# Kernel optimization log

Hardware: AMD Instinct MI355X
Metric: run time of the kernel (lower is better)

Reference implementation:

```python
import jax, jax.numpy as jnp
import numpy as np

B, M, D = 512, 96, 512
H = 8            # num_heads
DH = D // H      # head dim
NC = 3           # num_clusters
BETA = 5
MEM = 1024       # memory_size
EPS = 1e-8


def _l2norm(x, axis=-1):
    # torch F.cosine_similarity clamps each norm at eps=1e-8
    n = jnp.linalg.norm(x, axis=axis, keepdims=True)
    return x / jnp.maximum(n, EPS)


def _dynamic_clustering(sims):
    # sims: (B, M). Sort descending, split into NC equal groups,
    # per-group mean and (unbiased) std. (dynamic_clustering is not
    # defined in the source repo; this is the assumed implementation.)
    s = -jnp.sort(-sims, axis=1)               # descending
    g = s.reshape(B, NC, M // NC)
    means = g.mean(axis=-1)                    # (B, NC)
    stds = jnp.std(g, axis=-1, ddof=1)         # (B, NC)
    return means, stds


def setup_inputs() -> dict:
    key = jax.random.key(0)
    ks = jax.random.split(key, 6)
    vis_global = jax.random.normal(ks[0], (B, D), dtype=jnp.float32)
    text_features = jax.random.normal(ks[1], (B, M, D), dtype=jnp.float32)
    scale = 1.0 / np.sqrt(D)
    in_proj_w = jax.random.normal(ks[2], (3 * D, D), dtype=jnp.float32) * scale
    in_proj_b = jnp.zeros((3 * D,), dtype=jnp.float32)
    out_proj_w = jax.random.normal(ks[3], (D, D), dtype=jnp.float32) * scale
    out_proj_b = jnp.zeros((D,), dtype=jnp.float32)
    text_memory = jax.random.normal(ks[4], (MEM, D), dtype=jnp.float32)
    tau_p_log = jnp.log(jnp.asarray(0.1, dtype=jnp.float32))
    tau_n_log = jnp.log(jnp.asarray(0.05, dtype=jnp.float32))
    return dict(vis_global=vis_global, text_features=text_features,
                in_proj_w=in_proj_w, in_proj_b=in_proj_b,
                out_proj_w=out_proj_w, out_proj_b=out_proj_b,
                text_memory=text_memory, tau_p_log=tau_p_log, tau_n_log=tau_n_log)


def reference(vis_global, text_features, in_proj_w, in_proj_b,
              out_proj_w, out_proj_b, text_memory, tau_p_log, tau_n_log):
    # --- dynamic clustering over visual-text cosine sims ---
    sims = jnp.einsum('bd,bmd->bm', _l2norm(vis_global), _l2norm(text_features))
    means, stds = _dynamic_clustering(sims)
    cluster_scores = means / (stds + 1e-6)     # (B, NC)

    # --- MultiheadAttention: 1-token query, M-token key/value ---
    wq, wk, wv = in_proj_w[:D], in_proj_w[D:2 * D], in_proj_w[2 * D:]
    bq, bk, bv = in_proj_b[:D], in_proj_b[D:2 * D], in_proj_b[2 * D:]
    q = (vis_global @ wq.T + bq).reshape(B, H, DH)              # (B,H,DH)
    k = (text_features @ wk.T + bk).reshape(B, M, H, DH)        # (B,M,H,DH)
    v = (text_features @ wv.T + bv).reshape(B, M, H, DH)
    attn = jax.nn.softmax(jnp.einsum('bhd,bmhd->bhm', q, k) / np.sqrt(DH), axis=-1)
    ctx = jnp.einsum('bhm,bmhd->bhd', attn, v).reshape(B, D)
    corrected = ctx @ out_proj_w.T + out_proj_b                 # (B, D)

    tau_p = jnp.exp(tau_p_log)
    tau_n = jnp.exp(tau_n_log)
    pos_sim = jnp.sum(_l2norm(vis_global) * _l2norm(corrected), axis=-1)  # (B,)

    # memory-bank scatter (ptr starts at 0) + negatives, all detached
    corr_sg = jax.lax.stop_gradient(corrected)
    mem = text_memory.at[0:B].set(corr_sg)
    all_negs = jnp.concatenate([jnp.roll(corr_sg, 1, axis=0), mem], axis=0)  # (B+MEM, D)

    neg_sims = _l2norm(vis_global) @ _l2norm(all_negs).T        # (B, B+MEM)
    hard_negs, _ = jax.lax.top_k(neg_sims, BETA)                # (B, BETA)

    pos_term = jnp.exp(pos_sim / tau_p)
    neg_terms = jnp.exp(hard_negs / tau_n).sum(axis=1)
    loss = -jnp.mean(jnp.log(pos_term / (pos_term + neg_terms + 1e-8)))
    return loss, corrected, cluster_scores
```

## Files before the change

kernel.cpp:

```cpp
#include <hip/hip_runtime.h>
#include <math.h>

typedef unsigned short u16;
typedef unsigned int u32;
typedef __attribute__((ext_vector_type(8))) short short8;
typedef __attribute__((ext_vector_type(8))) _Float16 half8;
typedef __attribute__((ext_vector_type(4))) float f32x4;

#define EPS 1e-8f

__device__ inline float bf2f(u16 u) {
    union { u32 i; float f; } v; v.i = ((u32)u) << 16; return v.f;
}
__device__ inline u16 f2bf(float f) {
    union { float f; u32 u; } v; v.f = f;
    u32 r = v.u + 0x7fffu + ((v.u >> 16) & 1u);
    return (u16)(r >> 16);
}
__device__ inline u16 f2h(float f) {
    _Float16 h = (_Float16)f;
    union { _Float16 hh; u16 u; } v; v.hh = h; return v.u;
}
__device__ inline u32 pack2(float a, float b) {
    return (u32)f2bf(a) | ((u32)f2bf(b) << 16);
// ... 11 lines not shown
    #pragma unroll
    for (int kk = 0; kk < 16; kk++) {
        int c = c0 + kk * 32;
        *(uint4*)&As[srow * 520 + c] = *(const uint4*)&Ag[(size_t)srow * lda + c];
    }
}
__device__ __forceinline__ void mfma_k512(const u16* __restrict__ As,
                                          const u16* __restrict__ Bs,
                                          f32x4 (&acc)[2][2]) {
    const int t = threadIdx.x, lane = t & 63, w = t >> 6;
    const int wm = (w >> 1) * 32, wn = (w & 1) * 32;
    const int l16 = lane & 15, quad = lane >> 4;
    #pragma unroll
    for (int ks = 0; ks < 16; ks++) {
        short8 af[2], bfr[2];
        #pragma unroll
        for (int i = 0; i < 2; i++)
            af[i] = *(const short8*)&As[(wm + i * 16 + l16) * 520 + ks * 32 + quad * 8];
        #pragma unroll
        for (int j = 0; j < 2; j++)
            bfr[j] = *(const short8*)&Bs[(wn + j * 16 + l16) * 520 + ks * 32 + quad * 8];
        #pragma unroll
        for (int i = 0; i < 2; i++)
            #pragma unroll
            for (int j = 0; j < 2; j++)
                acc[i][j] = __builtin_amdgcn_mfma_f32_16x16x32_bf16(af[i], bfr[j], acc[i][j], 0, 0, 0);
    }
}

__global__ __launch_bounds__(256) void prep(const float* __restrict__ vis,
                                            const float* __restrict__ ipw,
                                            const float* __restrict__ opw,
                                            const float* __restrict__ tm,
                                            float* __restrict__ vis_n,
                                            u16* __restrict__ vis_nb,
                                            u16* __restrict__ vis_b,
                                            u16* __restrict__ wqb,
                                            u16* __restrict__ wvb,
                                            u16* __restrict__ wob,
                                            u16* __restrict__ negsb,
                                            u16* __restrict__ wkT,
                                            u16* __restrict__ woT,
                                            float* __restrict__ corrSS,
                                            float* __restrict__ loss0)
{
    int bid = blockIdx.x;
    int t = threadIdx.x;
    if (bid >= 1088) {
        __shared__ __align__(16) u16 T[64 * 72];
        int idx = bid - 1088;
        int a = idx >> 3, cb = idx & 7;
        int r = t >> 2, c0 = (t & 3) * 16;
        #pragma unroll
        for (int q = 0; q < 4; q++) {
            float4 v = *(const float4*)&opw[(size_t)(a * 64 + r) * 512 + cb * 64 + c0 + q * 4];
            T[(c0 + q * 4 + 0) * 72 + r] = f2bf(v.x);
            T[(c0 + q * 4 + 1) * 72 + r] = f2bf(v.y);
            T[(c0 + q * 4 + 2) * 72 + r] = f2bf(v.z);
            T[(c0 + q * 4 + 3) * 72 + r] = f2bf(v.w);
        }
        __syncthreads();
        int j = t >> 2, ch = (t & 3) * 16;
        *(uint4*)&woT[(size_t)(cb * 64 + j) * 512 + a * 64 + ch]     = *(const uint4*)&T[j * 72 + ch];
        *(uint4*)&woT[(size_t)(cb * 64 + j) * 512 + a * 64 + ch + 8] = *(const uint4*)&T[j * 72 + ch + 8];
        return;
    }
    if (bid >= 1024) {
        __shared__ __align__(16) u16 T[64 * 72];
        int idx = bid - 1024;
        int a = idx >> 3, cb = idx & 7;
        const float* wk = ipw + 262144;
        int r = t >> 2, c0 = (t & 3) * 16;
        #pragma unroll
        for (int q = 0; q < 4; q++) {
            float4 v = *(const float4*)&wk[(size_t)(a * 64 + r) * 512 + cb * 64 + c0 + q * 4];
            T[(c0 + q * 4 + 0) * 72 + r] = f2h(v.x);
            T[(c0 + q * 4 + 1) * 72 + r] = f2h(v.y);
            T[(c0 + q * 4 + 2) * 72 + r] = f2h(v.z);
            T[(c0 + q * 4 + 3) * 72 + r] = f2h(v.w);
        }
        __syncthreads();
        int j = t >> 2, ch = (t & 3) * 16;
        *(uint4*)&wkT[(size_t)(cb * 64 + j) * 512 + a * 64 + ch]     = *(const uint4*)&T[j * 72 + ch];
        *(uint4*)&wkT[(size_t)(cb * 64 + j) * 512 + a * 64 + ch + 8] = *(const uint4*)&T[j * 72 + ch + 8];
        return;
    }
    if (bid >= 896) {
        int wave = t >> 6, lane = t & 63;
        int j = 512 + (bid - 896) * 4 + wave;
        const float* row = tm + (size_t)(j - 512) * 512 + lane * 8;
        float4 x0 = *(const float4*)row;
        float4 x1 = *(const float4*)(row + 4);
        float ss = x0.x*x0.x + x0.y*x0.y + x0.z*x0.z + x0.w*x0.w
                 + x1.x*x1.x + x1.y*x1.y + x1.z*x1.z + x1.w*x1.w;
        ss = wave_sum(ss);
        float inv = 1.0f / fmaxf(sqrtf(ss), EPS);
        uint4 pk;
        pk.x = pack2(x0.x*inv, x0.y*inv); pk.y = pack2(x0.z*inv, x0.w*inv);
        pk.z = pack2(x1.x*inv, x1.y*inv); pk.w = pack2(x1.z*inv, x1.w*inv);
        *(uint4*)(negsb + (size_t)j * 512 + lane * 8) = pk;
        return;
    }
    if (bid >= 128) {
        int i = ((bid - 128) * 256 + t) * 4;
        const float* src; u16* dst; int j;
        if (i < 262144)      { j = i;          src = ipw + j;          dst = wqb + j; }
        else if (i < 524288) { j = i - 262144; src = ipw + 524288 + j; dst = wvb + j; }
        else                 { j = i - 524288; src = opw + j;          dst = wob + j; }
        float4 v = *(const float4*)src;
        uint2 pk; pk.x = pack2(v.x, v.y); pk.y = pack2(v.z, v.w);
        *(uint2*)dst = pk;
        return;
    }
    if (bid == 0) {
        if (t == 0) loss0[0] = 0.0f;
        corrSS[t] = 0.0f;
        corrSS[t + 256] = 0.0f;
    }
    int wave = t >> 6, lane = t & 63;
    int b = bid * 4 + wave;
    const float* row = vis + (size_t)b * 512 + lane * 8;
    float4 x0 = *(const float4*)row;
    float4 x1 = *(const float4*)(row + 4);
    uint4 rk;
    rk.x = pack2(x0.x, x0.y); rk.y = pack2(x0.z, x0.w);
    rk.z = pack2(x1.x, x1.y); rk.w = pack2(x1.z, x1.w);
    *(uint4*)(vis_b + (size_t)b * 512 + lane * 8) = rk;
    float ss = x0.x*x0.x + x0.y*x0.y + x0.z*x0.z + x0.w*x0.w
             + x1.x*x1.x + x1.y*x1.y + x1.z*x1.z + x1.w*x1.w;
    ss = wave_sum(ss);
    float inv = 1.0f / fmaxf(sqrtf(ss), EPS);
    float4 y0, y1;
    y0.x = x0.x*inv; y0.y = x0.y*inv; y0.z = x0.z*inv; y0.w = x0.w*inv;
    y1.x = x1.x*inv; y1.y = x1.y*inv; y1.z = x1.z*inv; y1.w = x1.w*inv;
    *(float4*)(vis_n + (size_t)b * 512 + lane * 8)     = y0;
    *(float4*)(vis_n + (size_t)b * 512 + lane * 8 + 4) = y1;
    uint4 pk;
    pk.x = pack2(y0.x, y0.y); pk.y = pack2(y0.z, y0.w);
    pk.z = pack2(y1.x, y1.y); pk.w = pack2(y1.z, y1.w);
    *(uint4*)(vis_nb + (size_t)b * 512 + lane * 8) = pk;
}

__global__ __launch_bounds__(256) void mid(const u16* __restrict__ visb,
                                           const u16* __restrict__ vis_nb,
                                           const u16* __restrict__ wqb,
                                           const float* __restrict__ ipb,
                                           const u16* __restrict__ wkT,
                                           u16* __restrict__ qkb,
                                           const u16* __restrict__ negsb,
                                           float* __restrict__ ns,
                                           const u16* __restrict__ woT,
                                           u16* __restrict__ G,
                                           const float* __restrict__ opb,
                                           float* __restrict__ vb,
                                           const float* __restrict__ vis_n)
{
    __shared__ __align__(16) u16 SM[3 * 64 * 72];
    const int bid = blockIdx.x;
    const int t = threadIdx.x, lane = t & 63, w = t >> 6;

    if (bid >= 192) {
        int idx = bid - 192;
        #pragma unroll 2
        for (int k = 0; k < 16; k++) {
            int b = idx * 64 + w * 16 + k;
            const float* vn = vis_n + (size_t)b * 512 + lane * 8;
            float4 a = *(const float4*)vn, c = *(const float4*)(vn + 4);
            const float* bo = opb + lane * 8;
            float4 b0 = *(const float4*)bo, b1 = *(const float4*)(bo + 4);
            float dt = a.x*b0.x + a.y*b0.y + a.z*b0.z + a.w*b0.w
                     + c.x*b1.x + c.y*b1.y + c.z*b1.z + c.w*b1.w;
            dt = wave_sum(dt);
            if (lane == 0) vb[b] = dt;
        }
        return;
    }

    const int wm = (w >> 1) * 32, wn = (w & 1) * 32;
    const int l16 = lane & 15, quad = lane >> 4;
    const int srow = t >> 3, scol = (t & 7) * 8;

    if (bid >= 64) {
        u16* As = SM;
        u16* Bs = SM + 4608;
        bool isG = (bid >= 128);
        int idx = bid - (isG ? 128 : 64);
        int m0 = (idx & 7) * 64, n0 = (idx >> 3) * 64;
        const u16* Bsrc = isG ? (woT + (size_t)n0 * 512)
                              : (negsb + (size_t)(512 + n0) * 512);
        f32x4 acc[2][2];
        for (int i = 0; i < 2; i++)
            for (int j = 0; j < 2; j++)
                for (int e = 0; e < 4; e++) acc[i][j][e] = 0.f;
        for (int ko = 0; ko < 512; ko += 64) {
            __syncthreads();
            #pragma unroll
            for (int i = 0; i < 2; i++) {
                int row = i * 32 + srow;
                *(uint4*)&As[row * 72 + scol] = *(const uint4*)&vis_nb[(size_t)(m0 + row) * 512 + ko + scol];
                *(uint4*)&Bs[row * 72 + scol] = *(const uint4*)&Bsrc[(size_t)row * 512 + ko + scol];
            }
            __syncthreads();
            #pragma unroll
            for (int ks = 0; ks < 2; ks++) {
                short8 af[2], bfr[2];
                #pragma unroll
                for (int i = 0; i < 2; i++)
                    af[i] = *(const short8*)&As[(wm + i * 16 + l16) * 72 + ks * 32 + quad * 8];
                #pragma unroll
                for (int j = 0; j < 2; j++)
                    bfr[j] = *(const short8*)&Bs[(wn + j * 16 + l16) * 72 + ks * 32 + quad * 8];
                #pragma unroll
                for (int i = 0; i < 2; i++)
                    #pragma unroll
                    for (int j = 0; j < 2; j++)
                        acc[i][j] = __builtin_amdgcn_mfma_f32_16x16x32_bf16(af[i], bfr[j], acc[i][j], 0, 0, 0);
            }
        }
        #pragma unroll
        for (int i = 0; i < 2; i++)
            #pragma unroll
            for (int j = 0; j < 2; j++)
                #pragma unroll
                for (int r = 0; r < 4; r++) {
                    int row = m0 + wm + i * 16 + quad * 4 + r;
                    int col = n0 + wn + j * 16 + l16;
                    if (isG) G[(size_t)row * 512 + col] = f2bf(acc[i][j][r]);
                    else     ns[(size_t)row * 1024 + 512 + col] = acc[i][j][r];
                }
        return;
    }

    u16* As = SM;
    u16* Bs = SM + 4608;
    u16* Qf = SM + 9216;
    const int m0 = (bid & 7) * 64, h = bid >> 3;

    f32x4 acc[2][2];
    for (int i = 0; i < 2; i++)
        for (int j = 0; j < 2; j++)
            for (int e = 0; e < 4; e++) acc[i][j][e] = 0.f;

    for (int ko = 0; ko < 512; ko += 64) {
        __syncthreads();
        #pragma unroll
        for (int i = 0; i < 2; i++) {
            int row = i * 32 + srow;
            *(uint4*)&As[row * 72 + scol] = *(const uint4*)&visb[(size_t)(m0 + row) * 512 + ko + scol];
            *(uint4*)&Bs[row * 72 + scol] = *(const uint4*)&wqb[(size_t)(h * 64 + row) * 512 + ko + scol];
        }
        __syncthreads();
        #pragma unroll
        for (int ks = 0; ks < 2; ks++) {
            short8 af[2], bfr[2];
            #pragma unroll
            for (int i = 0; i < 2; i++)
                af[i] = *(const short8*)&As[(wm + i * 16 + l16) * 72 + ks * 32 + quad * 8];
            #pragma unroll
            for (int j = 0; j < 2; j++)
                bfr[j] = *(const short8*)&Bs[(wn + j * 16 + l16) * 72 + ks * 32 + quad * 8];
            #pragma unroll
            for (int i = 0; i < 2; i++)
                #pragma unroll
                for (int j = 0; j < 2; j++)
                    acc[i][j] = __builtin_amdgcn_mfma_f32_16x16x32_bf16(af[i], bfr[j], acc[i][j], 0, 0, 0);
        }
    }
    #pragma unroll
    for (int i = 0; i < 2; i++)
        #pragma unroll
        for (int j = 0; j < 2; j++)
            #pragma unroll
            for (int r = 0; r < 4; r++) {
                int rl = wm + i * 16 + quad * 4 + r;
                int cl = wn + j * 16 + l16;
                Qf[rl * 72 + cl] = f2h(acc[i][j][r] + ipb[h * 64 + cl]);
            }
    for (int jt = 0; jt < 8; jt++) {
        __syncthreads();
        #pragma unroll
        for (int i = 0; i < 2; i++) {
            int row = i * 32 + srow;
            *(uint4*)&Bs[row * 72 + scol] = *(const uint4*)&wkT[(size_t)(jt * 64 + row) * 512 + h * 64 + scol];
        }
        __syncthreads();
        f32x4 a2[2][2];
        for (int i = 0; i < 2; i++)
            for (int j = 0; j < 2; j++)
                for (int e = 0; e < 4; e++) a2[i][j][e] = 0.f;
        #pragma unroll
        for (int ks = 0; ks < 2; ks++) {
            half8 af[2], bfr[2];
            #pragma unroll
            for (int i = 0; i < 2; i++)
                af[i] = *(const half8*)&Qf[(wm + i * 16 + l16) * 72 + ks * 32 + quad * 8];
            #pragma unroll
            for (int j = 0; j < 2; j++)
                bfr[j] = *(const half8*)&Bs[(wn + j * 16 + l16) * 72 + ks * 32 + quad * 8];
            #pragma unroll
            for (int i = 0; i < 2; i++)
                #pragma unroll
                for (int j = 0; j < 2; j++)
                    a2[i][j] = __builtin_amdgcn_mfma_f32_16x16x32_f16(af[i], bfr[j], a2[i][j], 0, 0, 0);
        }
        #pragma unroll
        for (int i = 0; i < 2; i++)
            #pragma unroll
            for (int j = 0; j < 2; j++)
                #pragma unroll
                for (int r = 0; r < 4; r++) {
                    int rb = m0 + wm + i * 16 + quad * 4 + r;
                    int cj = jt * 64 + wn + j * 16 + l16;
                    qkb[((size_t)rb * 8 + h) * 512 + cj] = f2bf(a2[i][j][r]);
                }
    }
}

__global__ __launch_bounds__(1024) void attn(const float* __restrict__ tf,
                                             const float* __restrict__ vis_n,
                                             const u16* __restrict__ qkb,
                                             u16* __restrict__ u_allb,
                                             float* __restrict__ out_cs)
{
    __shared__ __align__(16) u16 Xs[96 * 520];
    __shared__ __align__(16) u16 Qs[16 * 520];
    __shared__ __align__(16) u16 Ps[16 * 104];
    __shared__ float Sc[16 * 100];
    __shared__ float sm_[96], srt[96], linv[8];

    const int b = blockIdx.x;
    const int t = threadIdx.x, w = t >> 6, lane = t & 63;
    const int l16 = lane & 15, quad = lane >> 4;

    const float4* v4 = (const float4*)(vis_n + (size_t)b * 512 + lane * 8);
    float4 va = v4[0], vbv = v4[1];

    #pragma unroll
    for (int i = 0; i < 3; i++) {
        int m0r = w + i * 32;
        int m1r = m0r + 16;
        const float4* pa = (const float4*)(tf + ((size_t)b * 96 + m0r) * 512 + lane * 8);
        const float4* pb = (const float4*)(tf + ((size_t)b * 96 + m1r) * 512 + lane * 8);
        float4 a0 = pa[0], c0 = pa[1];
        float4 a1 = pb[0], c1 = pb[1];
        float ss0 = a0.x*a0.x + a0.y*a0.y + a0.z*a0.z + a0.w*a0.w
                  + c0.x*c0.x + c0.y*c0.y + c0.z*c0.z + c0.w*c0.w;
        float dt0 = a0.x*va.x + a0.y*va.y + a0.z*va.z + a0.w*va.w
                  + c0.x*vbv.x + c0.y*vbv.y + c0.z*vbv.z + c0.w*vbv.w;
        float ss1 = a1.x*a1.x + a1.y*a1.y + a1.z*a1.z + a1.w*a1.w
                  + c1.x*c1.x + c1.y*c1.y + c1.z*c1.z + c1.w*c1.w;
        float dt1 = a1.x*va.x + a1.y*va.y + a1.z*va.z + a1.w*va.w
                  + c1.x*vbv.x + c1.y*vbv.y + c1.z*vbv.z + c1.w*vbv.w;
        #pragma unroll
        for (int off = 32; off; off >>= 1) {
            ss0 += __shfl_xor(ss0, off, 64);
            dt0 += __shfl_xor(dt0, off, 64);
            ss1 += __shfl_xor(ss1, off, 64);
            dt1 += __shfl_xor(dt1, off, 64);
        }
        if (lane == 0) {
            sm_[m0r] = dt0 / fmaxf(sqrtf(ss0), EPS);
            sm_[m1r] = dt1 / fmaxf(sqrtf(ss1), EPS);
        }
        uint4 pk0, pk1;
        pk0.x = pack2(a0.x, a0.y); pk0.y = pack2(a0.z, a0.w);
        pk0.z = pack2(c0.x, c0.y); pk0.w = pack2(c0.z, c0.w);
        pk1.x = pack2(a1.x, a1.y); pk1.y = pack2(a1.z, a1.w);
        pk1.z = pack2(c1.x, c1.y); pk1.w = pack2(c1.z, c1.w);
        *(uint4*)&Xs[m0r * 520 + lane * 8] = pk0;
        *(uint4*)&Xs[m1r * 520 + lane * 8] = pk1;
    }
    if (w < 8) {
        *(uint4*)&Qs[w * 520 + lane * 8] = *(const uint4*)(qkb + ((size_t)b * 8 + w) * 512 + lane * 8);
    } else {
        uint4 z; z.x = 0; z.y = 0; z.z = 0; z.w = 0;
        *(uint4*)&Qs[w * 520 + lane * 8] = z;
    }
    __syncthreads();

    if (w < 6) {
        f32x4 acc;
        for (int e = 0; e < 4; e++) acc[e] = 0.f;
        #pragma unroll
        for (int ks = 0; ks < 16; ks++) {
            short8 a = *(const short8*)&Xs[(w * 16 + l16) * 520 + ks * 32 + quad * 8];
            short8 q = *(const short8*)&Qs[l16 * 520 + ks * 32 + quad * 8];
            acc = __builtin_amdgcn_mfma_f32_16x16x32_bf16(a, q, acc, 0, 0, 0);
        }
        #pragma unroll
        for (int r = 0; r < 4; r++)
            Sc[l16 * 100 + w * 16 + quad * 4 + r] = acc[r] * 0.125f;
    }
    __syncthreads();

    if (w < 8) {
        float e0 = __expf(Sc[w * 100 + lane]);
        float e1 = (lane < 32) ? __expf(Sc[w * 100 + 64 + lane]) : 0.f;
        float l = wave_sum(e0 + e1);
        Ps[w * 104 + lane] = f2bf(e0);
        if (lane < 32) Ps[w * 104 + 64 + lane] = f2bf(e1);
        if (lane == 0) linv[w] = 1.0f / l;
    } else {
        Ps[w * 104 + lane] = 0;
        if (lane < 40) Ps[w * 104 + 64 + lane] = 0;
    }
    if (t < 96) {
        float v = sm_[t]; int r = 0;
        for (int j = 0; j < 96; j++) {
            float u = sm_[j];
            r += (u > v) || (u == v && j < t);
        }
        srt[r] = v;
    }
    __syncthreads();

    #pragma unroll
    for (int jj = 0; jj < 2; jj++) {
        int n0 = (w * 2 + jj) * 16;
        f32x4 acc;
        for (int e = 0; e < 4; e++) acc[e] = 0.f;
        #pragma unroll
        for (int ks = 0; ks < 3; ks++) {
            short8 ap = *(const short8*)&Ps[l16 * 104 + ks * 32 + quad * 8];
            short8 bx;
            #pragma unroll
            for (int j = 0; j < 8; j++)
                bx[j] = (short)Xs[(ks * 32 + quad * 8 + j) * 520 + n0 + l16];
            acc = __builtin_amdgcn_mfma_f32_16x16x32_bf16(ap, bx, acc, 0, 0, 0);
        }
        if (quad < 2) {
            #pragma unroll
            for (int r = 0; r < 4; r++) {
                int h = quad * 4 + r;
                u_allb[((size_t)b * 8 + h) * 512 + n0 + l16] = f2bf(acc[r] * linv[h]);
            }
        }
    }
    if (t < 3) {
        float mean = 0.f;
        #pragma unroll 8
        for (int i = 0; i < 32; i++) mean += srt[t * 32 + i];
        mean *= (1.0f / 32.0f);
        float var = 0.f;
        #pragma unroll 8
        for (int i = 0; i < 32; i++) { float d = srt[t * 32 + i] - mean; var += d * d; }
        var *= (1.0f / 31.0f);
        out_cs[b * 3 + t] = mean / (sqrtf(var) + 1e-6f);
    }
}

__global__ __launch_bounds__(256) void ghead(const u16* __restrict__ u_allb,
                                             const u16* __restrict__ wvb,
                                             const float* __restrict__ bv,
                                             u16* __restrict__ ctxb)
{
    __shared__ __align__(16) u16 As[64 * 520];
    __shared__ __align__(16) u16 Bs[64 * 520];
    const int bid = blockIdx.x;
    const int m0 = (bid & 7) * 64, h = bid >> 3;
    const int t = threadIdx.x, lane = t & 63, w = t >> 6;
    const int wm = (w >> 1) * 32, wn = (w & 1) * 32;
    const int l16 = lane & 15, quad = lane >> 4;

    f32x4 acc[2][2];
    for (int i = 0; i < 2; i++)
        for (int j = 0; j < 2; j++)
            for (int e = 0; e < 4; e++) acc[i][j][e] = 0.f;

    stage64x512(u_allb + (size_t)m0 * 4096 + (size_t)h * 512, 4096, As);
    stage64x512(wvb + (size_t)h * 64 * 512, 512, Bs);
    __syncthreads();
    mfma_k512(As, Bs, acc);

    for (int i = 0; i < 2; i++) {
        int row = m0 + wm + i * 16 + quad * 4;
        for (int j = 0; j < 2; j++) {
            int col = wn + j * 16 + l16;
            float bb = bv[h * 64 + col];
            for (int r = 0; r < 4; r++)
                ctxb[(size_t)(row + r) * 512 + h * 64 + col] = f2bf(acc[i][j][r] + bb);
        }
    }
}

__global__ __launch_bounds__(256) void tail2(const u16* __restrict__ ctxb,
                                             const u16* __restrict__ wob,
                                             const float* __restrict__ bias,
                                             float* __restrict__ Cf,
                                             float* __restrict__ corrSS,
                                             const u16* __restrict__ G,
                                             const float* __restrict__ vb,
                                             float* __restrict__ ns)
{
    __shared__ __align__(16) u16 As[64 * 520];
    __shared__ __align__(16) u16 Bs[64 * 520];
    const int bid = blockIdx.x;
    const int t = threadIdx.x, lane = t & 63, w = t >> 6;
    const int wm = (w >> 1) * 32, wn = (w & 1) * 32;
    const int l16 = lane & 15, quad = lane >> 4;

    f32x4 acc[2][2];
    for (int i = 0; i < 2; i++)
        for (int j = 0; j < 2; j++)
            for (int e = 0; e < 4; e++) acc[i][j][e] = 0.f;

    if (bid < 64) {
        const int m0 = (bid & 7) * 64, n0 = (bid >> 3) * 64;
        stage64x512(ctxb + (size_t)m0 * 512, 512, As);
        stage64x512(wob + (size_t)n0 * 512, 512, Bs);
        __syncthreads();
        mfma_k512(As, Bs, acc);
        #pragma unroll
        for (int i = 0; i < 2; i++) {
// ... 111 lines not shown
        }
        if (lane == 0) {
            float pos = ns[(size_t)b * 1024 + b] * invn[b];
            float tp = expf(tau_p_log[0]);
            float p = expf(pos / tp);
            float term = logf(p / (p + nsum + 1e-8f));
            atomicAdd(out_loss, -term * (1.0f / 512.0f));
        }
    }
}

extern "C" void kernel_launch(void* const* d_in, const int* in_sizes, int n_in,
                              void* d_out, int out_size, void* d_ws, size_t ws_size,
                              hipStream_t stream) {
    const float* vis = (const float*)d_in[0];
    const float* tf  = (const float*)d_in[1];
    const float* ipw = (const float*)d_in[2];
    const float* ipb = (const float*)d_in[3];
    const float* opw = (const float*)d_in[4];
    const float* opb = (const float*)d_in[5];
    const float* tm  = (const float*)d_in[6];
    const float* tpl = (const float*)d_in[7];
    const float* tnl = (const float*)d_in[8];

    float* out       = (float*)d_out;
    float* out_loss  = out;
    float* out_corr  = out + 1;
    float* out_cs    = out + 1 + 512 * 512;

    char* p = (char*)d_ws;
    auto alloc = [&](size_t bytes) { char* r = p; p += (bytes + 255) & ~(size_t)255; return r; };
    float* vis_n  = (float*)alloc(512 * 512 * 4);
    u16*   vis_nb = (u16*)  alloc(512 * 512 * 2);
    u16*   vis_b  = (u16*)  alloc(512 * 512 * 2);
    u16*   wqb    = (u16*)  alloc(512 * 512 * 2);
    u16*   wvb    = (u16*)  alloc(512 * 512 * 2);
    u16*   wob    = (u16*)  alloc(512 * 512 * 2);
    u16*   wkT    = (u16*)  alloc(512 * 512 * 2);
    u16*   woT    = (u16*)  alloc(512 * 512 * 2);
    u16*   G      = (u16*)  alloc(512 * 512 * 2);
    u16*   qkb    = (u16*)  alloc((size_t)512 * 8 * 512 * 2);
    u16*   u_allb = (u16*)  alloc((size_t)512 * 8 * 512 * 2);
    u16*   ctxb   = (u16*)  alloc(512 * 512 * 2);
    u16*   negsb  = (u16*)  alloc(1024 * 512 * 2);
    float* ns     = (float*)alloc(512 * 1024 * 4);
    float* corrSS = (float*)alloc(512 * 4);
    float* vb     = (float*)alloc(512 * 4);

    const float* bv = ipb + 2 * 512;

    prep<<<1152, 256, 0, stream>>>(vis, ipw, opw, tm, vis_n, vis_nb, vis_b,
                                   wqb, wvb, wob, negsb, wkT, woT, corrSS, out_loss);
    mid<<<200, 256, 0, stream>>>(vis_b, vis_nb, wqb, ipb, wkT, qkb, negsb, ns,
                                 woT, G, opb, vb, vis_n);
    attn<<<512, 1024, 0, stream>>>(tf, vis_n, qkb, u_allb, out_cs);
    ghead<<<64, 256, 0, stream>>>(u_allb, wvb, bv, ctxb);
    tail2<<<128, 256, 0, stream>>>(ctxb, wob, opb, out_corr, corrSS, G, vb, ns);
    topk_loss<<<512, 256, 0, stream>>>(ns, corrSS, tpl, tnl, out_loss);
}
```

Before: 224.6 us.

## Fuse q/qk projection into prep and merge ghead with mid into one kernel

```diff
diff --git a/kernel.cpp b/kernel.cpp
--- a/kernel.cpp
+++ b/kernel.cpp
@@ -67,23 +67,23 @@
                                             const float* __restrict__ ipw,
                                             const float* __restrict__ opw,
                                             const float* __restrict__ tm,
+                                            const float* __restrict__ ipb,
                                             float* __restrict__ vis_n,
                                             u16* __restrict__ vis_nb,
-                                            u16* __restrict__ vis_b,
-                                            u16* __restrict__ wqb,
                                             u16* __restrict__ wvb,
                                             u16* __restrict__ wob,
                                             u16* __restrict__ negsb,
-                                            u16* __restrict__ wkT,
                                             u16* __restrict__ woT,
+                                            u16* __restrict__ qkb,
                                             float* __restrict__ corrSS,
                                             float* __restrict__ loss0)
 {
+    __shared__ __align__(16) u16 SMEM[3 * 64 * 72];
     int bid = blockIdx.x;
     int t = threadIdx.x;
-    if (bid >= 1088) {
-        __shared__ __align__(16) u16 T[64 * 72];
-        int idx = bid - 1088;
+    if (bid >= 832) {
+        u16* T = SMEM;
+        int idx = bid - 832;
         int a = idx >> 3, cb = idx & 7;
         int r = t >> 2, c0 = (t & 3) * 16;
         #pragma unroll
@@ -100,29 +100,9 @@
         *(uint4*)&woT[(size_t)(cb * 64 + j) * 512 + a * 64 + ch + 8] = *(const uint4*)&T[j * 72 + ch + 8];
         return;
     }
-    if (bid >= 1024) {
-        __shared__ __align__(16) u16 T[64 * 72];
-        int idx = bid - 1024;
-        int a = idx >> 3, cb = idx & 7;
-        const float* wk = ipw + 262144;
-        int r = t >> 2, c0 = (t & 3) * 16;
-        #pragma unroll
-        for (int q = 0; q < 4; q++) {
-            float4 v = *(const float4*)&wk[(size_t)(a * 64 + r) * 512 + cb * 64 + c0 + q * 4];
-            T[(c0 + q * 4 + 0) * 72 + r] = f2h(v.x);
-            T[(c0 + q * 4 + 1) * 72 + r] = f2h(v.y);
-            T[(c0 + q * 4 + 2) * 72 + r] = f2h(v.z);
-            T[(c0 + q * 4 + 3) * 72 + r] = f2h(v.w);
-        }
-        __syncthreads();
-        int j = t >> 2, ch = (t & 3) * 16;
-        *(uint4*)&wkT[(size_t)(cb * 64 + j) * 512 + a * 64 + ch]     = *(const uint4*)&T[j * 72 + ch];
-        *(uint4*)&wkT[(size_t)(cb * 64 + j) * 512 + a * 64 + ch + 8] = *(const uint4*)&T[j * 72 + ch + 8];
-        return;
-    }
-    if (bid >= 896) {
+    if (bid >= 704) {
         int wave = t >> 6, lane = t & 63;
-        int j = 512 + (bid - 896) * 4 + wave;
+        int j = 512 + (bid - 704) * 4 + wave;
         const float* row = tm + (size_t)(j - 512) * 512 + lane * 8;
         float4 x0 = *(const float4*)row;
         float4 x1 = *(const float4*)(row + 4);
@@ -136,63 +116,303 @@
         *(uint4*)(negsb + (size_t)j * 512 + lane * 8) = pk;
         return;
     }
-    if (bid >= 128) {
-        int i = ((bid - 128) * 256 + t) * 4;
-        const float* src; u16* dst; int j;
-        if (i < 262144)      { j = i;          src = ipw + j;          dst = wqb + j; }
-        else if (i < 524288) { j = i - 262144; src = ipw + 524288 + j; dst = wvb + j; }
-        else                 { j = i - 524288; src = opw + j;          dst = wob + j; }
-        float4 v = *(const float4*)src;
+    if (bid >= 448) {
+        int i = (bid - 448) * 1024 + t * 4;
+        float4 v = *(const float4*)(opw + i);
         uint2 pk; pk.x = pack2(v.x, v.y); pk.y = pack2(v.z, v.w);
-        *(uint2*)dst = pk;
-        return;
-    }
-    if (bid == 0) {
-        if (t == 0) loss0[0] = 0.0f;
-        corrSS[t] = 0.0f;
-        corrSS[t + 256] = 0.0f;
-    }
-    int wave = t >> 6, lane = t & 63;
-    int b = bid * 4 + wave;
-    const float* row = vis + (size_t)b * 512 + lane * 8;
-    float4 x0 = *(const float4*)row;
-    float4 x1 = *(const float4*)(row + 4);
-    uint4 rk;
-    rk.x = pack2(x0.x, x0.y); rk.y = pack2(x0.z, x0.w);
-    rk.z = pack2(x1.x, x1.y); rk.w = pack2(x1.z, x1.w);
-    *(uint4*)(vis_b + (size_t)b * 512 + lane * 8) = rk;
-    float ss = x0.x*x0.x + x0.y*x0.y + x0.z*x0.z + x0.w*x0.w
-             + x1.x*x1.x + x1.y*x1.y + x1.z*x1.z + x1.w*x1.w;
-    ss = wave_sum(ss);
-    float inv = 1.0f / fmaxf(sqrtf(ss), EPS);
-    float4 y0, y1;
-    y0.x = x0.x*inv; y0.y = x0.y*inv; y0.z = x0.z*inv; y0.w = x0.w*inv;
-    y1.x = x1.x*inv; y1.y = x1.y*inv; y1.z = x1.z*inv; y1.w = x1.w*inv;
-    *(float4*)(vis_n + (size_t)b * 512 + lane * 8)     = y0;
-    *(float4*)(vis_n + (size_t)b * 512 + lane * 8 + 4) = y1;
-    uint4 pk;
-    pk.x = pack2(y0.x, y0.y); pk.y = pack2(y0.z, y0.w);
-    pk.z = pack2(y1.x, y1.y); pk.w = pack2(y1.z, y1.w);
-    *(uint4*)(vis_nb + (size_t)b * 512 + lane * 8) = pk;
-}
-
-__global__ __launch_bounds__(256) void mid(const u16* __restrict__ visb,
-                                           const u16* __restrict__ vis_nb,
-                                           const u16* __restrict__ wqb,
-                                           const float* __restrict__ ipb,
-                                           const u16* __restrict__ wkT,
-                                           u16* __restrict__ qkb,
-                                           const u16* __restrict__ negsb,
-                                           float* __restrict__ ns,
-                                           const u16* __restrict__ woT,
-                                           u16* __restrict__ G,
-                                           const float* __restrict__ opb,
-                                           float* __restrict__ vb,
-                                           const float* __restrict__ vis_n)
+        *(uint2*)(wob + i) = pk;
+        return;
+    }
+    if (bid >= 192) {
+        int i = (bid - 192) * 1024 + t * 4;
+        float4 v = *(const float4*)(ipw + 524288 + i);
+        uint2 pk; pk.x = pack2(v.x, v.y); pk.y = pack2(v.z, v.w);
+        *(uint2*)(wvb + i) = pk;
+        return;
+    }
+    if (bid >= 64) {
+        if (bid == 64) {
+            if (t == 0) loss0[0] = 0.0f;
+            corrSS[t] = 0.0f;
+            corrSS[t + 256] = 0.0f;
+        }
+        int wave = t >> 6, lane = t & 63;
+        int b = (bid - 64) * 4 + wave;
+        const float* row = vis + (size_t)b * 512 + lane * 8;
+        float4 x0 = *(const float4*)row;
+        float4 x1 = *(const float4*)(row + 4);
+        float ss = x0.x*x0.x + x0.y*x0.y + x0.z*x0.z + x0.w*x0.w
+                 + x1.x*x1.x + x1.y*x1.y + x1.z*x1.z + x1.w*x1.w;
+        ss = wave_sum(ss);
+        float inv = 1.0f / fmaxf(sqrtf(ss), EPS);
+        float4 y0, y1;
+        y0.x = x0.x*inv; y0.y = x0.y*inv; y0.z = x0.z*inv; y0.w = x0.w*inv;
+        y1.x = x1.x*inv; y1.y = x1.y*inv; y1.z = x1.z*inv; y1.w = x1.w*inv;
+        *(float4*)(vis_n + (size_t)b * 512 + lane * 8)     = y0;
+        *(float4*)(vis_n + (size_t)b * 512 + lane * 8 + 4) = y1;
+        uint4 pk;
+        pk.x = pack2(y0.x, y0.y); pk.y = pack2(y0.z, y0.w);
+        pk.z = pack2(y1.x, y1.y); pk.w = pack2(y1.z, y1.w);
+        *(uint4*)(vis_nb + (size_t)b * 512 + lane * 8) = pk;
+        return;
+    }
+
+    u16* As = SMEM;
+    u16* Bs = SMEM + 4608;
+    u16* Qf = SMEM + 9216;
+    const int lane = t & 63, w = t >> 6;
+    const int wm = (w >> 1) * 32, wn = (w & 1) * 32;
+    const int l16 = lane & 15, quad = lane >> 4;
+    const int srow = t >> 3, scol = (t & 7) * 8;
+    const int m0 = (bid & 7) * 64, h = bid >> 3;
+    const float* wkf = ipw + 262144;
+
+    f32x4 acc[2][2];
+    for (int i = 0; i < 2; i++)
+        for (int j = 0; j < 2; j++)
+            for (int e = 0; e < 4; e++) acc[i][j][e] = 0.f;
+
+    for (int ko = 0; ko < 512; ko += 64) {
+        __syncthreads();
+        #pragma unroll
+        for (int i = 0; i < 2; i++) {
+            int row = i * 32 + srow;
+            const float* ap = vis + (size_t)(m0 + row) * 512 + ko + scol;
+            float4 a0 = *(const float4*)ap, a1 = *(const float4*)(ap + 4);
+            uint4 pkA;
+            pkA.x = pack2(a0.x, a0.y); pkA.y = pack2(a0.z, a0.w);
+            pkA.z = pack2(a1.x, a1.y); pkA.w = pack2(a1.z, a1.w);
+            *(uint4*)&As[row * 72 + scol] = pkA;
+            const float* bp = ipw + (size_t)(h * 64 + row) * 512 + ko + scol;
+            float4 b0 = *(const float4*)bp, b1 = *(const float4*)(bp + 4);
+            uint4 pkB;
+            pkB.x = pack2(b0.x, b0.y); pkB.y = pack2(b0.z, b0.w);
+            pkB.z = pack2(b1.x, b1.y); pkB.w = pack2(b1.z, b1.w);
+            *(uint4*)&Bs[row * 72 + scol] = pkB;
+        }
+        __syncthreads();
+        #pragma unroll
+        for (int ks = 0; ks < 2; ks++) {
+            short8 af[2], bfr[2];
+            #pragma unroll
+            for (int i = 0; i < 2; i++)
+                af[i] = *(const short8*)&As[(wm + i * 16 + l16) * 72 + ks * 32 + quad * 8];
+            #pragma unroll
+            for (int j = 0; j < 2; j++)
+                bfr[j] = *(const short8*)&Bs[(wn + j * 16 + l16) * 72 + ks * 32 + quad * 8];
+            #pragma unroll
+            for (int i = 0; i < 2; i++)
+                #pragma unroll
+                for (int j = 0; j < 2; j++)
+                    acc[i][j] = __builtin_amdgcn_mfma_f32_16x16x32_bf16(af[i], bfr[j], acc[i][j], 0, 0, 0);
+        }
+    }
+    #pragma unroll
+    for (int i = 0; i < 2; i++)
+        #pragma unroll
+        for (int j = 0; j < 2; j++)
+            #pragma unroll
+            for (int r = 0; r < 4; r++) {
+                int rl = wm + i * 16 + quad * 4 + r;
+                int cl = wn + j * 16 + l16;
+                Qf[rl * 72 + cl] = f2h(acc[i][j][r] + ipb[h * 64 + cl]);
+            }
+    for (int jt = 0; jt < 8; jt++) {
+        __syncthreads();
+        {
+            int r = t >> 2, c0 = (t & 3) * 16;
+            #pragma unroll
+            for (int q = 0; q < 4; q++) {
+                float4 v = *(const float4*)&wkf[(size_t)(h * 64 + r) * 512 + jt * 64 + c0 + q * 4];
+                Bs[(c0 + q * 4 + 0) * 72 + r] = f2h(v.x);
+                Bs[(c0 + q * 4 + 1) * 72 + r] = f2h(v.y);
+                Bs[(c0 + q * 4 + 2) * 72 + r] = f2h(v.z);
+                Bs[(c0 + q * 4 + 3) * 72 + r] = f2h(v.w);
+            }
+        }
+        __syncthreads();
+        f32x4 a2[2][2];
+        for (int i = 0; i < 2; i++)
+            for (int j = 0; j < 2; j++)
+                for (int e = 0; e < 4; e++) a2[i][j][e] = 0.f;
+        #pragma unroll
+        for (int ks = 0; ks < 2; ks++) {
+            half8 af[2], bfr[2];
+            #pragma unroll
+            for (int i = 0; i < 2; i++)
+                af[i] = *(const half8*)&Qf[(wm + i * 16 + l16) * 72 + ks * 32 + quad * 8];
+            #pragma unroll
+            for (int j = 0; j < 2; j++)
+                bfr[j] = *(const half8*)&Bs[(wn + j * 16 + l16) * 72 + ks * 32 + quad * 8];
+            #pragma unroll
+            for (int i = 0; i < 2; i++)
+                #pragma unroll
+                for (int j = 0; j < 2; j++)
+                    a2[i][j] = __builtin_amdgcn_mfma_f32_16x16x32_f16(af[i], bfr[j], a2[i][j], 0, 0, 0);
+        }
+        #pragma unroll
+        for (int i = 0; i < 2; i++)
+            #pragma unroll
+            for (int j = 0; j < 2; j++)
+                #pragma unroll
+                for (int r = 0; r < 4; r++) {
+                    int rb = m0 + wm + i * 16 + quad * 4 + r;
+                    int cj = jt * 64 + wn + j * 16 + l16;
+                    qkb[((size_t)rb * 8 + h) * 512 + cj] = f2bf(a2[i][j][r]);
+                }
+    }
+}
+
+__global__ __launch_bounds__(1024) void attn(const float* __restrict__ tf,
+                                             const float* __restrict__ vis_n,
+                                             const u16* __restrict__ qkb,
+                                             u16* __restrict__ u_allb,
+                                             float* __restrict__ out_cs)
 {
-    __shared__ __align__(16) u16 SM[3 * 64 * 72];
+    __shared__ __align__(16) u16 Xs[96 * 520];
+    __shared__ __align__(16) u16 Qs[16 * 520];
+    __shared__ __align__(16) u16 Ps[16 * 104];
+    __shared__ float Sc[16 * 100];
+    __shared__ float sm_[96], srt[96], linv[8];
+
+    const int b = blockIdx.x;
+    const int t = threadIdx.x, w = t >> 6, lane = t & 63;
+    const int l16 = lane & 15, quad = lane >> 4;
+
+    if (w < 8) {
+        *(uint4*)&Qs[w * 520 + lane * 8] = *(const uint4*)(qkb + ((size_t)b * 8 + w) * 512 + lane * 8);
+    } else {
+        uint4 z; z.x = 0; z.y = 0; z.z = 0; z.w = 0;
+        *(uint4*)&Qs[w * 520 + lane * 8] = z;
+    }
+    const float4* v4 = (const float4*)(vis_n + (size_t)b * 512 + lane * 8);
+    float4 va = v4[0], vbv = v4[1];
+
+    float4 xr[6][2];
+    #pragma unroll
+    for (int i = 0; i < 6; i++) {
+        const float4* pa = (const float4*)(tf + ((size_t)b * 96 + w + i * 16) * 512 + lane * 8);
+        xr[i][0] = pa[0];
+        xr[i][1] = pa[1];
+    }
+    float ssv[6], dtv[6];
+    #pragma unroll
+    for (int i = 0; i < 6; i++) {
+        float4 a = xr[i][0], c = xr[i][1];
+        ssv[i] = a.x*a.x + a.y*a.y + a.z*a.z + a.w*a.w
+               + c.x*c.x + c.y*c.y + c.z*c.z + c.w*c.w;
+        dtv[i] = a.x*va.x + a.y*va.y + a.z*va.z + a.w*va.w
+               + c.x*vbv.x + c.y*vbv.y + c.z*vbv.z + c.w*vbv.w;
+        uint4 pk;
+        pk.x = pack2(a.x, a.y); pk.y = pack2(a.z, a.w);
+        pk.z = pack2(c.x, c.y); pk.w = pack2(c.z, c.w);
+        *(uint4*)&Xs[(w + i * 16) * 520 + lane * 8] = pk;
+    }
+    #pragma unroll
+    for (int off = 32; off; off >>= 1) {
+        #pragma unroll
+        for (int i = 0; i < 6; i++) {
+            ssv[i] += __shfl_xor(ssv[i], off, 64);
+            dtv[i] += __shfl_xor(dtv[i], off, 64);
+        }
+    }
+    if (lane == 0) {
+        #pragma unroll
+        for (int i = 0; i < 6; i++)
+            sm_[w + i * 16] = dtv[i] / fmaxf(sqrtf(ssv[i]), EPS);
+    }
+    __syncthreads();
+
+    if (w < 6) {
+        f32x4 acc;
+        for (int e = 0; e < 4; e++) acc[e] = 0.f;
+        #pragma unroll
+        for (int ks = 0; ks < 16; ks++) {
+            short8 a = *(const short8*)&Xs[(w * 16 + l16) * 520 + ks * 32 + quad * 8];
+            short8 q = *(const short8*)&Qs[l16 * 520 + ks * 32 + quad * 8];
+            acc = __builtin_amdgcn_mfma_f32_16x16x32_bf16(a, q, acc, 0, 0, 0);
+        }
+        #pragma unroll
+        for (int r = 0; r < 4; r++)
+            Sc[l16 * 100 + w * 16 + quad * 4 + r] = acc[r] * 0.125f;
+    }
+    __syncthreads();
+
+    if (w < 8) {
+        float e0 = __expf(Sc[w * 100 + lane]);
+        float e1 = (lane < 32) ? __expf(Sc[w * 100 + 64 + lane]) : 0.f;
+        float l = wave_sum(e0 + e1);
+        Ps[w * 104 + lane] = f2bf(e0);
+        if (lane < 32) Ps[w * 104 + 64 + lane] = f2bf(e1);
+        if (lane == 0) linv[w] = 1.0f / l;
+    } else {
+        Ps[w * 104 + lane] = 0;
+        if (lane < 40) Ps[w * 104 + 64 + lane] = 0;
+    }
+    if (t < 96) {
+        float v = sm_[t]; int r = 0;
+        for (int j = 0; j < 96; j++) {
+            float u = sm_[j];
+            r += (u > v) || (u == v && j < t);
+        }
+        srt[r] = v;
+    }
+    __syncthreads();
+
+    #pragma unroll
+    for (int jj = 0; jj < 2; jj++) {
+        int n0 = (w * 2 + jj) * 16;
+        f32x4 acc;
+        for (int e = 0; e < 4; e++) acc[e] = 0.f;
+        #pragma unroll
+        for (int ks = 0; ks < 3; ks++) {
+            short8 ap = *(const short8*)&Ps[l16 * 104 + ks * 32 + quad * 8];
+            short8 bx;
+            #pragma unroll
+            for (int j = 0; j < 8; j++)
+                bx[j] = (short)Xs[(ks * 32 + quad * 8 + j) * 520 + n0 + l16];
+            acc = __builtin_amdgcn_mfma_f32_16x16x32_bf16(ap, bx, acc, 0, 0, 0);
+        }
+        if (quad < 2) {
+            #pragma unroll
+            for (int r = 0; r < 4; r++) {
+                int h = quad * 4 + r;
+                u_allb[((size_t)b * 8 + h) * 512 + n0 + l16] = f2bf(acc[r] * linv[h]);
+            }
+        }
+    }
+    if (t < 3) {
+        float mean = 0.f;
+        #pragma unroll 8
+        for (int i = 0; i < 32; i++) mean += srt[t * 32 + i];
+        mean *= (1.0f / 32.0f);
+        float var = 0.f;
+        #pragma unroll 8
+        for (int i = 0; i < 32; i++) { float d = srt[t * 32 + i] - mean; var += d * d; }
+        var *= (1.0f / 31.0f);
+        out_cs[b * 3 + t] = mean / (sqrtf(var) + 1e-6f);
+    }
+}
+
+__global__ __launch_bounds__(256) void gmid(const u16* __restrict__ u_allb,
+                                            const u16* __restrict__ wvb,
+                                            const float* __restrict__ bv,
+                                            u16* __restrict__ ctxb,
+                                            const u16* __restrict__ vis_nb,
+                                            const u16* __restrict__ negsb,
+                                            float* __restrict__ ns,
+                                            const u16* __restrict__ woT,
+                                            u16* __restrict__ G,
+                                            const float* __restrict__ opb,
+                                            float* __restrict__ vb,
+                                            const float* __restrict__ vis_n)
+{
+    __shared__ __align__(16) u16 As[64 * 520];
+    __shared__ __align__(16) u16 Bs[64 * 520];
     const int bid = blockIdx.x;
     const int t = threadIdx.x, lane = t & 63, w = t >> 6;
+    const int wm = (w >> 1) * 32, wn = (w & 1) * 32;
+    const int l16 = lane & 15, quad = lane >> 4;
 
     if (bid >= 192) {
         int idx = bid - 192;
@@ -211,309 +431,57 @@
         return;
     }
 
-    const int wm = (w >> 1) * 32, wn = (w & 1) * 32;
-    const int l16 = lane & 15, quad = lane >> 4;
-    const int srow = t >> 3, scol = (t & 7) * 8;
-
-    if (bid >= 64) {
-        u16* As = SM;
-        u16* Bs = SM + 4608;
-        bool isG = (bid >= 128);
-        int idx = bid - (isG ? 128 : 64);
-        int m0 = (idx & 7) * 64, n0 = (idx >> 3) * 64;
-        const u16* Bsrc = isG ? (woT + (size_t)n0 * 512)
-                              : (negsb + (size_t)(512 + n0) * 512);
-        f32x4 acc[2][2];
-        for (int i = 0; i < 2; i++)
-            for (int j = 0; j < 2; j++)
-                for (int e = 0; e < 4; e++) acc[i][j][e] = 0.f;
-        for (int ko = 0; ko < 512; ko += 64) {
-            __syncthreads();
-            #pragma unroll
-            for (int i = 0; i < 2; i++) {
-                int row = i * 32 + srow;
-                *(uint4*)&As[row * 72 + scol] = *(const uint4*)&vis_nb[(size_t)(m0 + row) * 512 + ko + scol];
-                *(uint4*)&Bs[row * 72 + scol] = *(const uint4*)&Bsrc[(size_t)row * 512 + ko + scol];
-            }
-            __syncthreads();
-            #pragma unroll
-            for (int ks = 0; ks < 2; ks++) {
-                short8 af[2], bfr[2];
-                #pragma unroll
-                for (int i = 0; i < 2; i++)
-                    af[i] = *(const short8*)&As[(wm + i * 16 + l16) * 72 + ks * 32 + quad * 8];
-                #pragma unroll
-                for (int j = 0; j < 2; j++)
-                    bfr[j] = *(const short8*)&Bs[(wn + j * 16 + l16) * 72 + ks * 32 + quad * 8];
-                #pragma unroll
-                for (int i = 0; i < 2; i++)
-                    #pragma unroll
-                    for (int j = 0; j < 2; j++)
-                        acc[i][j] = __builtin_amdgcn_mfma_f32_16x16x32_bf16(af[i], bfr[j], acc[i][j], 0, 0, 0);
-            }
-        }
-        #pragma unroll
-        for (int i = 0; i < 2; i++)
-            #pragma unroll
-            for (int j = 0; j < 2; j++)
-                #pragma unroll
-                for (int r = 0; r < 4; r++) {
-                    int row = m0 + wm + i * 16 + quad * 4 + r;
-                    int col = n0 + wn + j * 16 + l16;
-                    if (isG) G[(size_t)row * 512 + col] = f2bf(acc[i][j][r]);
-                    else     ns[(size_t)row * 1024 + 512 + col] = acc[i][j][r];
-                }
-        return;
-    }
-
-    u16* As = SM;
-    u16* Bs = SM + 4608;
-    u16* Qf = SM + 9216;
-    const int m0 = (bid & 7) * 64, h = bid >> 3;
-
     f32x4 acc[2][2];
     for (int i = 0; i < 2; i++)
         for (int j = 0; j < 2; j++)
             for (int e = 0; e < 4; e++) acc[i][j][e] = 0.f;
 
-    for (int ko = 0; ko < 512; ko += 64) {
-        __syncthreads();
-        #pragma unroll
+    if (bid < 64) {
+        const int m0 = (bid & 7) * 64, h = bid >> 3;
+        stage64x512(u_allb + (size_t)m0 * 4096 + (size_t)h * 512, 4096, As);
+        stage64x512(wvb + (size_t)h * 64 * 512, 512, Bs);
+        __syncthreads();
+        mfma_k512(As, Bs, acc);
         for (int i = 0; i < 2; i++) {
-            int row = i * 32 + srow;
-            *(uint4*)&As[row * 72 + scol] = *(const uint4*)&visb[(size_t)(m0 + row) * 512 + ko + scol];
-            *(uint4*)&Bs[row * 72 + scol] = *(const uint4*)&wqb[(size_t)(h * 64 + row) * 512 + ko + scol];
-        }
-        __syncthreads();
-        #pragma unroll
-        for (int ks = 0; ks < 2; ks++) {
-            short8 af[2], bfr[2];
-            #pragma unroll
-            for (int i = 0; i < 2; i++)
-                af[i] = *(const short8*)&As[(wm + i * 16 + l16) * 72 + ks * 32 + quad * 8];
-            #pragma unroll
-            for (int j = 0; j < 2; j++)
-                bfr[j] = *(const short8*)&Bs[(wn + j * 16 + l16) * 72 + ks * 32 + quad * 8];
-            #pragma unroll
-            for (int i = 0; i < 2; i++)
-                #pragma unroll
-                for (int j = 0; j < 2; j++)
-                    acc[i][j] = __builtin_amdgcn_mfma_f32_16x16x32_bf16(af[i], bfr[j], acc[i][j], 0, 0, 0);
-        }
-    }
-    #pragma unroll
-    for (int i = 0; i < 2; i++)
-        #pragma unroll
-        for (int j = 0; j < 2; j++)
-            #pragma unroll
-            for (int r = 0; r < 4; r++) {
-                int rl = wm + i * 16 + quad * 4 + r;
-                int cl = wn + j * 16 + l16;
-                Qf[rl * 72 + cl] = f2h(acc[i][j][r] + ipb[h * 64 + cl]);
+            int row = m0 + wm + i * 16 + quad * 4;
+            for (int j = 0; j < 2; j++) {
+                int col = wn + j * 16 + l16;
+                float bb = bv[h * 64 + col];
+                for (int r = 0; r < 4; r++)
+                    ctxb[(size_t)(row + r) * 512 + h * 64 + col] = f2bf(acc[i][j][r] + bb);
             }
-    for (int jt = 0; jt < 8; jt++) {
-        __syncthreads();
-        #pragma unroll
+        }
+        return;
+    }
+    if (bid < 128) {
+        const int idx = bid - 64;
+        const int m0 = (idx & 7) * 64, n0 = (idx >> 3) * 64;
+        stage64x512(vis_nb + (size_t)m0 * 512, 512, As);
+        stage64x512(negsb + (size_t)(512 + n0) * 512, 512, Bs);
+        __syncthreads();
+        mfma_k512(As, Bs, acc);
         for (int i = 0; i < 2; i++) {
-            int row = i * 32 + srow;
-            *(uint4*)&Bs[row * 72 + scol] = *(const uint4*)&wkT[(size_t)(jt * 64 + row) * 512 + h * 64 + scol];
-        }
-        __syncthreads();
-        f32x4 a2[2][2];
-        for (int i = 0; i < 2; i++)
-            for (int j = 0; j < 2; j++)
-                for (int e = 0; e < 4; e++) a2[i][j][e] = 0.f;
-        #pragma unroll
-        for (int ks = 0; ks < 2; ks++) {
-            half8 af[2], bfr[2];
-            #pragma unroll
-            for (int i = 0; i < 2; i++)
-                af[i] = *(const half8*)&Qf[(wm + i * 16 + l16) * 72 + ks * 32 + quad * 8];
-            #pragma unroll
-            for (int j = 0; j < 2; j++)
-                bfr[j] = *(const half8*)&Bs[(wn + j * 16 + l16) * 72 + ks * 32 + quad * 8];
-            #pragma unroll
-            for (int i = 0; i < 2; i++)
-                #pragma unroll
-                for (int j = 0; j < 2; j++)
-                    a2[i][j] = __builtin_amdgcn_mfma_f32_16x16x32_f16(af[i], bfr[j], a2[i][j], 0, 0, 0);
-        }
-        #pragma unroll
-        for (int i = 0; i < 2; i++)
-            #pragma unroll
-            for (int j = 0; j < 2; j++)
-                #pragma unroll
-                for (int r = 0; r < 4; r++) {
-                    int rb = m0 + wm + i * 16 + quad * 4 + r;
-                    int cj = jt * 64 + wn + j * 16 + l16;
-                    qkb[((size_t)rb * 8 + h) * 512 + cj] = f2bf(a2[i][j][r]);
-                }
-    }
-}
-
-__global__ __launch_bounds__(1024) void attn(const float* __restrict__ tf,
-                                             const float* __restrict__ vis_n,
-                                             const u16* __restrict__ qkb,
-                                             u16* __restrict__ u_allb,
-                                             float* __restrict__ out_cs)
-{
-    __shared__ __align__(16) u16 Xs[96 * 520];
-    __shared__ __align__(16) u16 Qs[16 * 520];
-    __shared__ __align__(16) u16 Ps[16 * 104];
-    __shared__ float Sc[16 * 100];
-    __shared__ float sm_[96], srt[96], linv[8];
-
-    const int b = blockIdx.x;
-    const int t = threadIdx.x, w = t >> 6, lane = t & 63;
-    const int l16 = lane & 15, quad = lane >> 4;
-
-    const float4* v4 = (const float4*)(vis_n + (size_t)b * 512 + lane * 8);
-    float4 va = v4[0], vbv = v4[1];
-
-    #pragma unroll
-    for (int i = 0; i < 3; i++) {
-        int m0r = w + i * 32;
-        int m1r = m0r + 16;
-        const float4* pa = (const float4*)(tf + ((size_t)b * 96 + m0r) * 512 + lane * 8);
-        const float4* pb = (const float4*)(tf + ((size_t)b * 96 + m1r) * 512 + lane * 8);
-        float4 a0 = pa[0], c0 = pa[1];
-        float4 a1 = pb[0], c1 = pb[1];
-        float ss0 = a0.x*a0.x + a0.y*a0.y + a0.z*a0.z + a0.w*a0.w
-                  + c0.x*c0.x + c0.y*c0.y + c0.z*c0.z + c0.w*c0.w;
-        float dt0 = a0.x*va.x + a0.y*va.y + a0.z*va.z + a0.w*va.w
-                  + c0.x*vbv.x + c0.y*vbv.y + c0.z*vbv.z + c0.w*vbv.w;
-        float ss1 = a1.x*a1.x + a1.y*a1.y + a1.z*a1.z + a1.w*a1.w
-                  + c1.x*c1.x + c1.y*c1.y + c1.z*c1.z + c1.w*c1.w;
-        float dt1 = a1.x*va.x + a1.y*va.y + a1.z*va.z + a1.w*va.w
-                  + c1.x*vbv.x + c1.y*vbv.y + c1.z*vbv.z + c1.w*vbv.w;
-        #pragma unroll
-        for (int off = 32; off; off >>= 1) {
-            ss0 += __shfl_xor(ss0, off, 64);
-            dt0 += __shfl_xor(dt0, off, 64);
-            ss1 += __shfl_xor(ss1, off, 64);
-            dt1 += __shfl_xor(dt1, off, 64);
-        }
-        if (lane == 0) {
-            sm_[m0r] = dt0 / fmaxf(sqrtf(ss0), EPS);
-            sm_[m1r] = dt1 / fmaxf(sqrtf(ss1), EPS);
-        }
-        uint4 pk0, pk1;
-        pk0.x = pack2(a0.x, a0.y); pk0.y = pack2(a0.z, a0.w);
-        pk0.z = pack2(c0.x, c0.y); pk0.w = pack2(c0.z, c0.w);
-        pk1.x = pack2(a1.x, a1.y); pk1.y = pack2(a1.z, a1.w);
-        pk1.z = pack2(c1.x, c1.y); pk1.w = pack2(c1.z, c1.w);
-        *(uint4*)&Xs[m0r * 520 + lane * 8] = pk0;
-        *(uint4*)&Xs[m1r * 520 + lane * 8] = pk1;
-    }
-    if (w < 8) {
-        *(uint4*)&Qs[w * 520 + lane * 8] = *(const uint4*)(qkb + ((size_t)b * 8 + w) * 512 + lane * 8);
-    } else {
-        uint4 z; z.x = 0; z.y = 0; z.z = 0; z.w = 0;
-        *(uint4*)&Qs[w * 520 + lane * 8] = z;
-    }
-    __syncthreads();
-
-    if (w < 6) {
-        f32x4 acc;
-        for (int e = 0; e < 4; e++) acc[e] = 0.f;
-        #pragma unroll
-        for (int ks = 0; ks < 16; ks++) {
-            short8 a = *(const short8*)&Xs[(w * 16 + l16) * 520 + ks * 32 + quad * 8];
-            short8 q = *(const short8*)&Qs[l16 * 520 + ks * 32 + quad * 8];
-            acc = __builtin_amdgcn_mfma_f32_16x16x32_bf16(a, q, acc, 0, 0, 0);
-        }
-        #pragma unroll
-        for (int r = 0; r < 4; r++)
-            Sc[l16 * 100 + w * 16 + quad * 4 + r] = acc[r] * 0.125f;
-    }
-    __syncthreads();
-
-    if (w < 8) {
-        float e0 = __expf(Sc[w * 100 + lane]);
-        float e1 = (lane < 32) ? __expf(Sc[w * 100 + 64 + lane]) : 0.f;
-        float l = wave_sum(e0 + e1);
-        Ps[w * 104 + lane] = f2bf(e0);
-        if (lane < 32) Ps[w * 104 + 64 + lane] = f2bf(e1);
-        if (lane == 0) linv[w] = 1.0f / l;
-    } else {
-        Ps[w * 104 + lane] = 0;
-        if (lane < 40) Ps[w * 104 + 64 + lane] = 0;
-    }
-    if (t < 96) {
-        float v = sm_[t]; int r = 0;
-        for (int j = 0; j < 96; j++) {
-            float u = sm_[j];
-            r += (u > v) || (u == v && j < t);
-        }
-        srt[r] = v;
-    }
-    __syncthreads();
-
-    #pragma unroll
-    for (int jj = 0; jj < 2; jj++) {
-        int n0 = (w * 2 + jj) * 16;
-        f32x4 acc;
-        for (int e = 0; e < 4; e++) acc[e] = 0.f;
-        #pragma unroll
-        for (int ks = 0; ks < 3; ks++) {
-            short8 ap = *(const short8*)&Ps[l16 * 104 + ks * 32 + quad * 8];
-            short8 bx;
-            #pragma unroll
-            for (int j = 0; j < 8; j++)
-                bx[j] = (short)Xs[(ks * 32 + quad * 8 + j) * 520 + n0 + l16];
-            acc = __builtin_amdgcn_mfma_f32_16x16x32_bf16(ap, bx, acc, 0, 0, 0);
-        }
-        if (quad < 2) {
-            #pragma unroll
-            for (int r = 0; r < 4; r++) {
-                int h = quad * 4 + r;
-                u_allb[((size_t)b * 8 + h) * 512 + n0 + l16] = f2bf(acc[r] * linv[h]);
+            int row = m0 + wm + i * 16 + quad * 4;
+            for (int j = 0; j < 2; j++) {
+                int col = 512 + n0 + wn + j * 16 + l16;
+                for (int r = 0; r < 4; r++)
+                    ns[(size_t)(row + r) * 1024 + col] = acc[i][j][r];
             }
         }
-    }
-    if (t < 3) {
-        float mean = 0.f;
-        #pragma unroll 8
-        for (int i = 0; i < 32; i++) mean += srt[t * 32 + i];
-        mean *= (1.0f / 32.0f);
-        float var = 0.f;
-        #pragma unroll 8
-        for (int i = 0; i < 32; i++) { float d = srt[t * 32 + i] - mean; var += d * d; }
-        var *= (1.0f / 31.0f);
-        out_cs[b * 3 + t] = mean / (sqrtf(var) + 1e-6f);
-    }
-}
-
-__global__ __launch_bounds__(256) void ghead(const u16* __restrict__ u_allb,
-                                             const u16* __restrict__ wvb,
-                                             const float* __restrict__ bv,
-                                             u16* __restrict__ ctxb)
-{
-    __shared__ __align__(16) u16 As[64 * 520];
-    __shared__ __align__(16) u16 Bs[64 * 520];
-    const int bid = blockIdx.x;
-    const int m0 = (bid & 7) * 64, h = bid >> 3;
-    const int t = threadIdx.x, lane = t & 63, w = t >> 6;
-    const int wm = (w >> 1) * 32, wn = (w & 1) * 32;
-    const int l16 = lane & 15, quad = lane >> 4;
-
-    f32x4 acc[2][2];
-    for (int i = 0; i < 2; i++)
-        for (int j = 0; j < 2; j++)
-            for (int e = 0; e < 4; e++) acc[i][j][e] = 0.f;
-
-    stage64x512(u_allb + (size_t)m0 * 4096 + (size_t)h * 512, 4096, As);
-    stage64x512(wvb + (size_t)h * 64 * 512, 512, Bs);
+        return;
+    }
+    const int idx = bid - 128;
+    const int m0 = (idx & 7) * 64, n0 = (idx >> 3) * 64;
+    stage64x512(vis_nb + (size_t)m0 * 512, 512, As);
+    stage64x512(woT + (size_t)n0 * 512, 512, Bs);
     __syncthreads();
     mfma_k512(As, Bs, acc);
-
     for (int i = 0; i < 2; i++) {
         int row = m0 + wm + i * 16 + quad * 4;
         for (int j = 0; j < 2; j++) {
-            int col = wn + j * 16 + l16;
-            float bb = bv[h * 64 + col];
+            int col = n0 + wn + j * 16 + l16;
             for (int r = 0; r < 4; r++)
-                ctxb[(size_t)(row + r) * 512 + h * 64 + col] = f2bf(acc[i][j][r] + bb);
+                G[(size_t)(row + r) * 512 + col] = f2bf(acc[i][j][r]);
         }
     }
 }
@@ -691,11 +659,8 @@
     auto alloc = [&](size_t bytes) { char* r = p; p += (bytes + 255) & ~(size_t)255; return r; };
     float* vis_n  = (float*)alloc(512 * 512 * 4);
     u16*   vis_nb = (u16*)  alloc(512 * 512 * 2);
-    u16*   vis_b  = (u16*)  alloc(512 * 512 * 2);
-    u16*   wqb    = (u16*)  alloc(512 * 512 * 2);
     u16*   wvb    = (u16*)  alloc(512 * 512 * 2);
     u16*   wob    = (u16*)  alloc(512 * 512 * 2);
-    u16*   wkT    = (u16*)  alloc(512 * 512 * 2);
     u16*   woT    = (u16*)  alloc(512 * 512 * 2);
     u16*   G      = (u16*)  alloc(512 * 512 * 2);
     u16*   qkb    = (u16*)  alloc((size_t)512 * 8 * 512 * 2);
@@ -708,12 +673,11 @@
 
     const float* bv = ipb + 2 * 512;
 
-    prep<<<1152, 256, 0, stream>>>(vis, ipw, opw, tm, vis_n, vis_nb, vis_b,
-                                   wqb, wvb, wob, negsb, wkT, woT, corrSS, out_loss);
-    mid<<<200, 256, 0, stream>>>(vis_b, vis_nb, wqb, ipb, wkT, qkb, negsb, ns,
-                                 woT, G, opb, vb, vis_n);
+    prep<<<896, 256, 0, stream>>>(vis, ipw, opw, tm, ipb, vis_n, vis_nb,
+                                  wvb, wob, negsb, woT, qkb, corrSS, out_loss);
     attn<<<512, 1024, 0, stream>>>(tf, vis_n, qkb, u_allb, out_cs);
-    ghead<<<64, 256, 0, stream>>>(u_allb, wvb, bv, ctxb);
+    gmid<<<200, 256, 0, stream>>>(u_allb, wvb, bv, ctxb, vis_nb, negsb, ns,
+                                  woT, G, opb, vb, vis_n);
     tail2<<<128, 256, 0, stream>>>(ctxb, wob, opb, out_corr, corrSS, G, vb, ns);
     topk_loss<<<512, 256, 0, stream>>>(ns, corrSS, tpl, tnl, out_loss);
 }
```

Result: slower. 238.6 us (+6.2%).
